# Optimization experiments

Hardware: AMD Instinct MI355X
Metric: run time of the kernel (lower is better)

The kernel has to match this reference:

```python
import jax, jax.numpy as jnp
import numpy as np

SOFTMAX = True
SPLAT = True


def setup_inputs() -> dict:
    key = jax.random.key(0)
    k1, k2 = jax.random.split(key)
    data = jax.random.normal(k1, (4, 3, 128, 128), dtype=jnp.float32)
    kernels = jax.random.normal(k2, (4, 441, 128, 128), dtype=jnp.float32)
    return {"data": data, "kernels": kernels}


def _scatter2gather(kern):
    # kern: [bs, k, k, h, w] splat kernels. Gather weight at pixel p for
    # neighbor offset d equals splat weight at pixel p+d for offset -d:
    #   gather[b,i,j,y,x] = splat[b, k-1-i, k-1-j, y+i-c, x+j-c]  (zero outside)
    bs, k, _, h, w = kern.shape
    c = k // 2
    flipped = kern[:, ::-1, ::-1]  # [bs,k,k,h,w]
    padded = jnp.pad(flipped, ((0, 0), (0, 0), (0, 0), (c, c), (c, c)))
    idx = jnp.arange(k)

    def slice_ij(i, j):
        plane = padded[:, i, j]  # [bs, h+2c, w+2c]
        return jax.lax.dynamic_slice(plane, (0, i, j), (bs, h, w))

    g = jax.vmap(lambda i: jax.vmap(lambda j: slice_ij(i, j))(idx))(idx)  # [k,k,bs,h,w]
    return jnp.transpose(g, (2, 0, 1, 3, 4))


def _kernel_weighting(data, kern):
    # out[b,c,y,x] = sum_ij kern[b,i,j,y,x] * data[b,c,y+i-cc,x+j-cc] (zero pad)
    # sum_w = same filtering applied to an all-ones tensor.
    bs, ch, h, w = data.shape
    k = kern.shape[1]
    cc = k // 2
    patches = jax.lax.conv_general_dilated_patches(
        data, (k, k), (1, 1), ((cc, cc), (cc, cc)))  # [bs, ch*k*k, h, w]
    patches = patches.reshape(bs, ch, k, k, h, w)
    out = jnp.einsum('bcijyx,bijyx->bcyx', patches, kern)
    # validity mask = zero-padded ones, separable in y/x
    ii = jnp.arange(k)
    yy = jnp.arange(h)
    xx = jnp.arange(w)
    py = yy[None, :] + ii[:, None] - cc  # [k,h]
    px = xx[None, :] + ii[:, None] - cc  # [k,w]
    vy = ((py >= 0) & (py < h))
    vx = ((px >= 0) & (px < w))
    valid = (vy[:, None, :, None] & vx[None, :, None, :]).astype(kern.dtype)  # [k,k,h,w]
    sum_w = jnp.einsum('bijyx,ijyx->byx', kern, valid)
    return out, sum_w


def reference(data, kernels):
    bs, k2, h, w = kernels.shape
    k = int(np.sqrt(k2))
    kern = kernels.reshape(bs, k, k, h, w)
    if SPLAT:
        kern = _scatter2gather(kern)
    if SOFTMAX:
        kern = jax.nn.softmax(kern.reshape(bs, k * k, h, w), axis=1)
        kern = kern.reshape(bs, k, k, h, w)
    out, sum_w = _kernel_weighting(data, kern)
    return out, sum_w[:, None]  # [bs,ch,h,w], [bs,1,h,w]
```

## Files before the change

kernel.cpp:

```cpp
#include <hip/hip_runtime.h>

#define KS 21
#define CC 10
#define H 128
#define W 128
#define HW (H*W)
#define NCH 3
#define B 4
#define PW (W + 2*CC)
#define S 7
#define CH 3

#define KT_BYTES (63*304)
#define DT_BYTES (CH*PW*16)
typedef _Float16 half4v __attribute__((ext_vector_type(4)));

__global__ __launch_bounds__(256, 4)
void kaw_part(const float* __restrict__ data,
              const float* __restrict__ kern,
              float* __restrict__ part)
{
    __shared__ __align__(16) unsigned char smem[KT_BYTES + DT_BYTES];
    unsigned char* ktB = smem;
    float*         dtF = (float*)(smem + KT_BYTES);

    const int tid  = threadIdx.x;
    const int x    = tid & 127;
    const int half = tid >> 7;
    const int y  = blockIdx.x;
    const int b  = blockIdx.y;
    const int i0 = blockIdx.z * CH;

    const float* __restrict__ kbase = kern + (size_t)b * (KS * KS) * HW;
    const float* __restrict__ dbase = data + (size_t)b * NCH * HW;

    #pragma unroll
    for (int k = 0; k < 8; ++k) {
        int idx = tid + k * 256;
        if (idx < 63 * 32) {
            int row = idx >> 5;
            int c4  = idx & 31;
            int ii  = row >= 42 ? 2 : (row >= 21 ? 1 : 0);
            int j   = row - ii * 21;
            int q   = (KS - 1 - (i0 + ii)) * KS + (KS - 1 - j);
            int py  = y + i0 + ii - CC;
            half4v hv = (half4v){(_Float16)0, (_Float16)0, (_Float16)0, (_Float16)0};
            if ((unsigned)py < (unsigned)H) {
                float4 g = *reinterpret_cast<const float4*>(
                    kbase + (size_t)q * HW + (size_t)py * W + c4 * 4);
                hv = (half4v){(_Float16)__expf(g.x), (_Float16)__expf(g.y),
                              (_Float16)__expf(g.z), (_Float16)__expf(g.w)};
            }
            *reinterpret_cast<half4v*>(ktB + row * 304 + 24 + c4 * 8) = hv;
        }
    }
    for (int p = tid; p < 63 * 12; p += 256) {
        int row = p / 12, k = p - row * 12;
        int off = row * 304 + (k < 6 ? k * 4 : 280 + (k - 6) * 4);
        *reinterpret_cast<unsigned*>(ktB + off) = 0u;
    }

    #pragma unroll
    for (int k = 0; k < 2; ++k) {
        int e = tid + k * 256;
        if (e < CH * PW) {
            int ii = e >= 2 * PW ? 2 : (e >= PW ? 1 : 0);
            int c  = e - ii * PW;
            int gy = y + i0 + ii - CC;
            int gx = c - CC;
            float4 v = make_float4(0.f, 0.f, 0.f, 0.f);
            if ((unsigned)gy < (unsigned)H && (unsigned)gx < (unsigned)W) {
                v.x = dbase[(0 * H + gy) * W + gx];
                v.y = dbase[(1 * H + gy) * W + gx];
                v.z = dbase[(2 * H + gy) * W + gx];
            }
            *reinterpret_cast<float4*>(dtF + e * 4) = v;
        }
    }
    __syncthreads();

    float acc0 = 0.f, acc1 = 0.f, acc2 = 0.f, accw = 0.f;
    const int jb = half ? 11 : 0;
    const int nj = half ? 10 : 11;
    #pragma unroll
    for (int ii = 0; ii < CH; ++ii) {
        const unsigned char* kp = ktB + (ii * 21 + jb) * 304 + 2 * jb + 4 + 2 * x;
        const unsigned char* dp = (const unsigned char*)dtF + ii * (PW * 16) + 16 * x;
        #pragma unroll 11
        for (int jj = 0; jj < nj; ++jj) {
            float e = (float)*reinterpret_cast<const _Float16*>(kp + jj * 306);
            float4 dv = *reinterpret_cast<const float4*>(dp + (jb + jj) * 16);
            acc0 += e * dv.x;
            acc1 += e * dv.y;
            acc2 += e * dv.z;
            accw += e;
        }
    }

    __syncthreads();
    float* sred = dtF;
    if (half == 1) {
        *reinterpret_cast<float4*>(sred + x * 4) = make_float4(acc0, acc1, acc2, accw);
    }
    __syncthreads();
    if (half == 0) {
        float4 s = *reinterpret_cast<const float4*>(sred + x * 4);
        acc0 += s.x; acc1 += s.y; acc2 += s.z; accw += s.w;
        float* p = part + (size_t)(blockIdx.z * B + b) * 4 * HW + (size_t)y * W + x;
        p[0]      = acc0;
        p[HW]     = acc1;
        p[2 * HW] = acc2;
        p[3 * HW] = accw;
    }
}

__global__ __launch_bounds__(256)
void kaw_reduce(const float* __restrict__ part,
                float* __restrict__ out,
                float* __restrict__ sumw)
{
    const int idx = blockIdx.x * 256 + threadIdx.x;
    const int b   = idx >> 14;
    const int px  = idx & (HW - 1);
    const int yy  = px >> 7;
    const int xx  = px & 127;

    float a0 = 0.f, a1 = 0.f, a2 = 0.f, aw = 0.f;
    #pragma unroll
    for (int s = 0; s < S; ++s) {
        const float* p = part + (size_t)(s * B + b) * 4 * HW + px;
        a0 += p[0];
        a1 += p[HW];
        a2 += p[2 * HW];
        aw += p[3 * HW];
    }
    int nry = max(0, CC - yy) + max(0, yy - (H - 1 - CC));
    int nrx = max(0, CC - xx) + max(0, xx - (W - 1 - CC));
    float cnt = 21.f * nry + (float)((21 - nry) * nrx);
    float inv = 1.0f / (aw + cnt);
    const size_t o = (size_t)b * NCH * HW + px;
    out[o]          = a0 * inv;
    out[o + HW]     = a1 * inv;
    out[o + 2 * HW] = a2 * inv;
    sumw[(size_t)b * HW + px] = aw * inv;
}

#define TY 2
__global__ __launch_bounds__(256)
void kaw_mono(const float* __restrict__ data,
              const float* __restrict__ kern,
              float* __restrict__ out,
              float* __restrict__ sumw)
{
    const int x  = threadIdx.x;
    const int ty = threadIdx.y;
    const int y0 = blockIdx.x * TY;
    const int b  = blockIdx.y;
    const int y  = y0 + ty;

    __shared__ __align__(16) float sdat[TY + 2 * CC][PW][4];

    const float* __restrict__ dbase = data + (size_t)b * NCH * HW;
    const int tid = ty * W + x;
    for (int e = tid; e < (TY + 2 * CC) * PW; e += W * TY) {
        int r  = e / PW;
        int xx = e - r * PW;
        int gy = y0 + r - CC;
        int gx = xx - CC;
        float4 v = make_float4(0.f, 0.f, 0.f, 0.f);
        if ((unsigned)gy < (unsigned)H && (unsigned)gx < (unsigned)W) {
            v.x = dbase[(0 * H + gy) * W + gx];
            v.y = dbase[(1 * H + gy) * W + gx];
            v.z = dbase[(2 * H + gy) * W + gx];
        }
        *reinterpret_cast<float4*>(&sdat[r][xx][0]) = v;
    }
    __syncthreads();

    const float* __restrict__ kbase = kern + (size_t)b * (KS * KS) * HW;
    float acc0 = 0.f, acc1 = 0.f, acc2 = 0.f, accw = 0.f, accd = 0.f;

    for (int i = 0; i < KS; ++i) {
        const int py = y + i - CC;
        if ((unsigned)py >= (unsigned)H) { accd += (float)KS; continue; }
        const float* __restrict__ krow =
            kbase + (size_t)(KS - 1 - i) * KS * HW + (size_t)py * W;
        const float* __restrict__ srow = &sdat[ty + i][0][0];
        #pragma unroll
        for (int j = 0; j < KS; ++j) {
            int px = x + j - CC;
            bool vx = (unsigned)px < (unsigned)W;
            int spx = px < 0 ? 0 : (px > W - 1 ? W - 1 : px);
            float g = krow[(size_t)(KS - 1 - j) * HW + spx];
            float e = vx ? __expf(g) : 0.f;
            float4 dv = *reinterpret_cast<const float4*>(srow + (size_t)(x + j) * 4);
            acc0 += e * dv.x; acc1 += e * dv.y; acc2 += e * dv.z;
            accw += e; accd += vx ? e : 1.f;
        }
    }

    const float inv = 1.0f / accd;
    const size_t o = (size_t)b * NCH * HW + (size_t)y * W + x;
    out[o]          = acc0 * inv;
    out[o + HW]     = acc1 * inv;
    out[o + 2 * HW] = acc2 * inv;
    sumw[(size_t)b * HW + (size_t)y * W + x] = accw * inv;
}

extern "C" void kernel_launch(void* const* d_in, const int* in_sizes, int n_in,
                              void* d_out, int out_size, void* d_ws, size_t ws_size,
                              hipStream_t stream)
{
    const float* data = (const float*)d_in[0];
    const float* kern = (const float*)d_in[1];
    float* out  = (float*)d_out;
    float* sumw = out + (size_t)B * NCH * HW;

    const size_t ws_need = (size_t)S * B * 4 * HW * sizeof(float);
    if (ws_size >= ws_need) {
        float* part = (float*)d_ws;
        dim3 g1(H, B, S);
        kaw_part<<<g1, 256, 0, stream>>>(data, kern, part);
        kaw_reduce<<<B * HW / 256, 256, 0, stream>>>(part, out, sumw);
    } else {
        dim3 g(H / TY, B), blk(W, TY);
        kaw_mono<<<g, blk, 0, stream>>>(data, kern, out, sumw);
    }
}
```

Baseline: 32.93 us.

## Store data tile in fp16 LDS, interleave partials as float4, raise occupancy

Stores the shared-memory data tile as half4 instead of float4, halving its LDS footprint and read bandwidth, and raises the launch-bounds occupancy hint from 4 to 6 blocks. Partial sums are written and read as interleaved float4 per pixel, so the reduce kernel does one vector load per slice instead of four strided scalar loads. Rounding input data to fp16 adds precision error to the weighted sums.

Result: no change. 33.03 us (+0.3%).

```diff
diff --git a/kernel.cpp b/kernel.cpp
--- a/kernel.cpp
+++ b/kernel.cpp
@@ -12,17 +12,17 @@
 #define CH 3
 
 #define KT_BYTES (63*304)
-#define DT_BYTES (CH*PW*16)
+#define DT_BYTES (CH*PW*8)
 typedef _Float16 half4v __attribute__((ext_vector_type(4)));
 
-__global__ __launch_bounds__(256, 4)
+__global__ __launch_bounds__(256, 6)
 void kaw_part(const float* __restrict__ data,
               const float* __restrict__ kern,
-              float* __restrict__ part)
+              float4* __restrict__ part)
 {
     __shared__ __align__(16) unsigned char smem[KT_BYTES + DT_BYTES];
     unsigned char* ktB = smem;
-    float*         dtF = (float*)(smem + KT_BYTES);
+    unsigned char* dtB = smem + KT_BYTES;
 
     const int tid  = threadIdx.x;
     const int x    = tid & 127;
@@ -68,13 +68,13 @@
             int c  = e - ii * PW;
             int gy = y + i0 + ii - CC;
             int gx = c - CC;
-            float4 v = make_float4(0.f, 0.f, 0.f, 0.f);
+            half4v v = (half4v){(_Float16)0, (_Float16)0, (_Float16)0, (_Float16)0};
             if ((unsigned)gy < (unsigned)H && (unsigned)gx < (unsigned)W) {
-                v.x = dbase[(0 * H + gy) * W + gx];
-                v.y = dbase[(1 * H + gy) * W + gx];
-                v.z = dbase[(2 * H + gy) * W + gx];
+                v.x = (_Float16)dbase[(0 * H + gy) * W + gx];
+                v.y = (_Float16)dbase[(1 * H + gy) * W + gx];
+                v.z = (_Float16)dbase[(2 * H + gy) * W + gx];
             }
-            *reinterpret_cast<float4*>(dtF + e * 4) = v;
+            *reinterpret_cast<half4v*>(dtB + e * 8) = v;
         }
     }
     __syncthreads();
@@ -82,23 +82,29 @@
     float acc0 = 0.f, acc1 = 0.f, acc2 = 0.f, accw = 0.f;
     const int jb = half ? 11 : 0;
     const int nj = half ? 10 : 11;
-    #pragma unroll
-    for (int ii = 0; ii < CH; ++ii) {
-        const unsigned char* kp = ktB + (ii * 21 + jb) * 304 + 2 * jb + 4 + 2 * x;
-        const unsigned char* dp = (const unsigned char*)dtF + ii * (PW * 16) + 16 * x;
-        #pragma unroll 11
-        for (int jj = 0; jj < nj; ++jj) {
-            float e = (float)*reinterpret_cast<const _Float16*>(kp + jj * 306);
-            float4 dv = *reinterpret_cast<const float4*>(dp + (jb + jj) * 16);
-            acc0 += e * dv.x;
-            acc1 += e * dv.y;
-            acc2 += e * dv.z;
-            accw += e;
-        }
-    }
-
-    __syncthreads();
-    float* sred = dtF;
+    {
+        const unsigned char* kp = ktB + 2 * x;
+        const unsigned char* dp = dtB + 8 * x;
+        #pragma unroll
+        for (int ii = 0; ii < CH; ++ii) {
+            #pragma unroll 11
+            for (int jj = 0; jj < nj; ++jj) {
+                const int j = jb + jj;
+                _Float16 e16 = *reinterpret_cast<const _Float16*>(
+                    kp + (ii * 21 + j) * 304 + 2 * j + 4);
+                half4v dv = *reinterpret_cast<const half4v*>(
+                    dp + ii * 1184 + j * 8);
+                float e = (float)e16;
+                acc0 += e * (float)dv.x;
+                acc1 += e * (float)dv.y;
+                acc2 += e * (float)dv.z;
+                accw += e;
+            }
+        }
+    }
+
+    __syncthreads();
+    float* sred = (float*)dtB;
     if (half == 1) {
         *reinterpret_cast<float4*>(sred + x * 4) = make_float4(acc0, acc1, acc2, accw);
     }
@@ -106,16 +112,13 @@
     if (half == 0) {
         float4 s = *reinterpret_cast<const float4*>(sred + x * 4);
         acc0 += s.x; acc1 += s.y; acc2 += s.z; accw += s.w;
-        float* p = part + (size_t)(blockIdx.z * B + b) * 4 * HW + (size_t)y * W + x;
-        p[0]      = acc0;
-        p[HW]     = acc1;
-        p[2 * HW] = acc2;
-        p[3 * HW] = accw;
+        part[(size_t)(blockIdx.z * B + b) * HW + (size_t)y * W + x] =
+            make_float4(acc0, acc1, acc2, accw);
     }
 }
 
 __global__ __launch_bounds__(256)
-void kaw_reduce(const float* __restrict__ part,
+void kaw_reduce(const float4* __restrict__ part,
                 float* __restrict__ out,
                 float* __restrict__ sumw)
 {
@@ -128,11 +131,11 @@
     float a0 = 0.f, a1 = 0.f, a2 = 0.f, aw = 0.f;
     #pragma unroll
     for (int s = 0; s < S; ++s) {
-        const float* p = part + (size_t)(s * B + b) * 4 * HW + px;
-        a0 += p[0];
-        a1 += p[HW];
-        a2 += p[2 * HW];
-        aw += p[3 * HW];
+        float4 p = part[(size_t)(s * B + b) * HW + px];
+        a0 += p.x;
+        a1 += p.y;
+        a2 += p.z;
+        aw += p.w;
     }
     int nry = max(0, CC - yy) + max(0, yy - (H - 1 - CC));
     int nrx = max(0, CC - xx) + max(0, xx - (W - 1 - CC));
@@ -216,9 +219,9 @@
     float* out  = (float*)d_out;
     float* sumw = out + (size_t)B * NCH * HW;
 
-    const size_t ws_need = (size_t)S * B * 4 * HW * sizeof(float);
+    const size_t ws_need = (size_t)S * B * HW * sizeof(float4);
     if (ws_size >= ws_need) {
-        float* part = (float*)d_ws;
+        float4* part = (float4*)d_ws;
         dim3 g1(H, B, S);
         kaw_part<<<g1, 256, 0, stream>>>(data, kern, part);
         kaw_reduce<<<B * HW / 256, 256, 0, stream>>>(part, out, sumw);
```
